# Kernel tuning notes

Hardware: AMD Instinct MI355X
Metric: run time of the kernel (lower is better)

Reference implementation:

```python
import jax, jax.numpy as jnp
import numpy as np

N_NODES = 50000
N_EDGES = 800000
D = 64
NUM_GRAPHS = 64


def gcn_conv(x, src, dst, deg_inv_sqrt, W, b):
    # GCNConv: h = X W; out_i = sum_{j->i} norm_ij * h_j + self-loop term + b
    h = x @ W  # [N, D_out]
    norm = deg_inv_sqrt[src] * deg_inv_sqrt[dst]  # [E]
    msgs = h[src] * norm[:, None]  # [E, D_out] -- dominant gather
    out = jax.ops.segment_sum(msgs, dst, num_segments=N_NODES)
    # self-loop edge (i,i) with norm = deg_i^-1
    out = out + h * (deg_inv_sqrt ** 2)[:, None]
    return out + b


def setup_inputs() -> dict:
    key = jax.random.key(0)
    ks = jax.random.split(key, 12)
    x = jax.random.normal(ks[0], (N_NODES, D), dtype=jnp.float32)
    edge_index = jax.random.randint(ks[1], (2, N_EDGES), 0, N_NODES, dtype=jnp.int64)
    batch = jnp.sort(jax.random.randint(ks[2], (N_NODES,), 0, NUM_GRAPHS, dtype=jnp.int64))
    s = 1.0 / np.sqrt(D)
    W1 = jax.random.uniform(ks[3], (D, D), jnp.float32, -s, s)
    b1 = jnp.zeros((D,), jnp.float32)
    W2 = jax.random.uniform(ks[4], (D, D), jnp.float32, -s, s)
    b2 = jnp.zeros((D,), jnp.float32)
    W3 = jax.random.uniform(ks[5], (D, D), jnp.float32, -s, s)
    b3 = jnp.zeros((D,), jnp.float32)
    Wl = jax.random.uniform(ks[6], (D, 1), jnp.float32, -s, s)
    bl = jnp.zeros((1,), jnp.float32)
    return {"x": x, "edge_index": edge_index, "batch": batch,
            "W1": W1, "b1": b1, "W2": W2, "b2": b2, "W3": W3, "b3": b3,
            "Wl": Wl, "bl": bl}


def reference(x, edge_index, batch, W1, b1, W2, b2, W3, b3, Wl, bl):
    src, dst = edge_index[0], edge_index[1]
    # symmetric GCN normalization with self-loops: deg_i = in_degree_i + 1
    deg = jax.ops.segment_sum(jnp.ones((N_EDGES,), x.dtype), dst, num_segments=N_NODES) + 1.0
    deg_inv_sqrt = deg ** -0.5
    h = jax.nn.relu(gcn_conv(x, src, dst, deg_inv_sqrt, W1, b1))
    h = jax.nn.relu(gcn_conv(h, src, dst, deg_inv_sqrt, W2, b2))
    h = jax.nn.relu(gcn_conv(h, src, dst, deg_inv_sqrt, W3, b3))
    # global mean pool over graphs
    sums = jax.ops.segment_sum(h, batch, num_segments=NUM_GRAPHS)  # [G, D]
    counts = jax.ops.segment_sum(jnp.ones((N_NODES,), h.dtype), batch, num_segments=NUM_GRAPHS)
    pooled = sums / jnp.clip(counts, 1.0)[:, None]
    return pooled @ Wl + bl  # [G, 1]
```

## Files before the change

kernel.cpp:

```cpp
#include <hip/hip_runtime.h>

#define N_NODES 50000
#define N_EDGES 800000
#define DIM 64
#define NUM_GRAPHS 64
#define NPART 8
#define PART_NODES 6250

typedef unsigned short u16;
typedef unsigned int u32;

__device__ __forceinline__ u16 bf16_rne(float f) {
  u32 u = __float_as_uint(f);
  u32 r = (u + 0x7fffu + ((u >> 16) & 1u)) >> 16;
  return (u16)r;
}

__global__ void init_kernel(int* __restrict__ cnt, float* __restrict__ partial,
                            const float* __restrict__ x, u16* __restrict__ xh) {
  int i = blockIdx.x * blockDim.x + threadIdx.x;
  if (i < N_NODES) cnt[i] = 0;
  if (i < NUM_GRAPHS) partial[i] = 0.f;
  int stride = gridDim.x * blockDim.x;
  for (int k = i; k < N_NODES * DIM / 4; k += stride) {
    float4 v = reinterpret_cast<const float4*>(x)[k];
    ushort4 o;
    o.x = bf16_rne(v.x); o.y = bf16_rne(v.y);
    o.z = bf16_rne(v.z); o.w = bf16_rne(v.w);
    reinterpret_cast<ushort4*>(xh)[k] = o;
  }
}

__global__ void pack_count_kernel(const int* __restrict__ src, const int* __restrict__ dst,
                                  u32* __restrict__ epk, int* __restrict__ cnt, int E) {
  int stride = gridDim.x * blockDim.x;
  for (int e = blockIdx.x * blockDim.x + threadIdx.x; e < E; e += stride) {
    int d = dst[e];
    int s = src[e];
    epk[e] = ((u32)s << 16) | (u32)d;
    atomicAdd(&cnt[d], 1);
  }
}

__global__ void scanA_kernel(const int* __restrict__ cnt, int* __restrict__ rowptr,
                             int* __restrict__ bsum, float* __restrict__ dis, int N) {
  __shared__ int wsum[16];
  int i = blockIdx.x * 1024 + threadIdx.x;
  int lane = threadIdx.x & 63, wid = threadIdx.x >> 6;
  int v = (i < N) ? cnt[i] : 0;
  if (i < N) dis[i] = rsqrtf((float)(v + 1));
  int sv = v;
  #pragma unroll
  for (int off = 1; off < 64; off <<= 1) {
    int t = __shfl_up(sv, off, 64);
    if (lane >= off) sv += t;
  }
  if (lane == 63) wsum[wid] = sv;
  __syncthreads();
  if (wid == 0) {
    int wv = (lane < 16) ? wsum[lane] : 0;
    #pragma unroll
    for (int off = 1; off < 16; off <<= 1) {
      int t = __shfl_up(wv, off, 64);
      if (lane >= off) wv += t;
    }
    if (lane < 16) wsum[lane] = wv;
  }
  __syncthreads();
  if (i < N) rowptr[i] = (wid ? wsum[wid - 1] : 0) + (sv - v);
  if (threadIdx.x == 1023) bsum[blockIdx.x] = wsum[15];
}

__global__ void scanC_kernel(int* __restrict__ rowptr, const int* __restrict__ bsum,
                             int* __restrict__ cursor, int nb, int N) {
  __shared__ int s_off;
  __shared__ int s_total;
  int b = blockIdx.x;
  if (threadIdx.x < 64) {
    int t = threadIdx.x;
    int v = (t < nb) ? bsum[t] : 0;
    #pragma unroll
    for (int off = 1; off < 64; off <<= 1) {
      int u = __shfl_up(v, off, 64);
      if (t >= off) v += u;
    }
    if (t == (b == 0 ? 0 : b - 1)) s_off = (b == 0) ? 0 : v;
    if (t == nb - 1) s_total = v;
  }
  __syncthreads();
  int i = b * 1024 + threadIdx.x;
  if (i < N) {
    int r = rowptr[i] + s_off;
    rowptr[i] = r;
    cursor[i] = r;
  }
  if (b == 0 && threadIdx.x == 0) rowptr[N] = s_total;
}

__global__ void fill_kernel(const u32* __restrict__ epk,
                            int* __restrict__ cursor, int* __restrict__ esrc, int E) {
  int p = blockIdx.x & 7;
  int lo = p * PART_NODES, hi = lo + PART_NODES;
  int stride = (gridDim.x >> 3) * blockDim.x;
  for (int e = (blockIdx.x >> 3) * blockDim.x + threadIdx.x; e < E; e += stride) {
    u32 rec = epk[e];
    int d = (int)(rec & 0xffffu);
    if (d >= lo && d < hi) {
      int pos = atomicAdd(&cursor[d], 1);
      esrc[pos] = (int)(rec >> 16);
    }
  }
}

#define UNPACK_FMA(q, d)                                              \
  a0 = fmaf(__uint_as_float((q).x << 16), (d), a0);                   \
  a1 = fmaf(__uint_as_float((q).x & 0xffff0000u), (d), a1);           \
  a2 = fmaf(__uint_as_float((q).y << 16), (d), a2);                   \
  a3 = fmaf(__uint_as_float((q).y & 0xffff0000u), (d), a3);           \
  a4 = fmaf(__uint_as_float((q).z << 16), (d), a4);                   \
  a5 = fmaf(__uint_as_float((q).z & 0xffff0000u), (d), a5);           \
  a6 = fmaf(__uint_as_float((q).w << 16), (d), a6);                   \
  a7 = fmaf(__uint_as_float((q).w & 0xffff0000u), (d), a7);

__global__ __launch_bounds__(256) void aggregate_kernel(const u16* __restrict__ Fh,
    const int* __restrict__ rowptr, const int* __restrict__ esrc,
    const float* __restrict__ dis, float* __restrict__ A, int N) {
  int node = blockIdx.x * 4 + (threadIdx.x >> 6);
  if (node >= N) return;
  int lane = threadIdx.x & 63;
  int qc = lane & 7;
  int qe = lane >> 3;
  const uint4* __restrict__ F8 = reinterpret_cast<const uint4*>(Fh);
  int beg = rowptr[node], end = rowptr[node + 1];
  float a0 = 0.f, a1 = 0.f, a2 = 0.f, a3 = 0.f;
  float a4 = 0.f, a5 = 0.f, a6 = 0.f, a7 = 0.f;
  int j = beg;
  for (; j + 16 <= end; j += 16) {
    int s0 = esrc[j + qe];
    int s1 = esrc[j + 8 + qe];
    float d0 = dis[s0], d1 = dis[s1];
    uint4 q0 = F8[(size_t)s0 * 8 + qc];
    uint4 q1 = F8[(size_t)s1 * 8 + qc];
    UNPACK_FMA(q0, d0)
    UNPACK_FMA(q1, d1)
  }
  if (j + 8 <= end) {
    int s0 = esrc[j + qe];
    float d0 = dis[s0];
    uint4 q0 = F8[(size_t)s0 * 8 + qc];
    UNPACK_FMA(q0, d0)
    j += 8;
  }
  if (j + qe < end) {
    int s0 = esrc[j + qe];
    float d0 = dis[s0];
    uint4 q0 = F8[(size_t)s0 * 8 + qc];
    UNPACK_FMA(q0, d0)
  }
  #pragma unroll
  for (int m = 8; m < 64; m <<= 1) {
    a0 += __shfl_xor(a0, m, 64); a1 += __shfl_xor(a1, m, 64);
    a2 += __shfl_xor(a2, m, 64); a3 += __shfl_xor(a3, m, 64);
    a4 += __shfl_xor(a4, m, 64); a5 += __shfl_xor(a5, m, 64);
    a6 += __shfl_xor(a6, m, 64); a7 += __shfl_xor(a7, m, 64);
  }
  if (qe == 0) {
    float dn = dis[node];
    uint4 qs = F8[(size_t)node * 8 + qc];
    float s0 = __uint_as_float(qs.x << 16), s1 = __uint_as_float(qs.x & 0xffff0000u);
    float s2 = __uint_as_float(qs.y << 16), s3 = __uint_as_float(qs.y & 0xffff0000u);
    float s4 = __uint_as_float(qs.z << 16), s5 = __uint_as_float(qs.z & 0xffff0000u);
    float s6 = __uint_as_float(qs.w << 16), s7 = __uint_as_float(qs.w & 0xffff0000u);
    float4 o0, o1;
    o0.x = (a0 + s0 * dn) * dn; o0.y = (a1 + s1 * dn) * dn;
    o0.z = (a2 + s2 * dn) * dn; o0.w = (a3 + s3 * dn) * dn;
    o1.x = (a4 + s4 * dn) * dn; o1.y = (a5 + s5 * dn) * dn;
    o1.z = (a6 + s6 * dn) * dn; o1.w = (a7 + s7 * dn) * dn;
    float4* A4 = reinterpret_cast<float4*>(A + (size_t)node * DIM + qc * 8);
    A4[0] = o0;
    A4[1] = o1;
  }
}

__global__ __launch_bounds__(256) void gemm_bias_relu(const float* __restrict__ X,
    const float* __restrict__ W, const float* __restrict__ b,
    u16* __restrict__ Fh, int N) {
  __shared__ float4 Xs[64][16];
  int col = threadIdx.x & 63, wid = threadIdx.x >> 6;
  float wreg[DIM];
  #pragma unroll
  for (int k = 0; k < DIM; ++k) wreg[k] = W[k * DIM + col];
  float bias = b[col];
  int row0 = blockIdx.x * 64;
  for (int i = threadIdx.x; i < 64 * 16; i += 256) {
    int r = i >> 4, c = i & 15;
    int gr = row0 + r;
    Xs[r][c] = (gr < N) ? reinterpret_cast<const float4*>(X)[(size_t)gr * 16 + c]
                        : make_float4(0.f, 0.f, 0.f, 0.f);
  }
  __syncthreads();
  for (int rr = 0; rr < 16; ++rr) {
    int lr = wid * 16 + rr;
    int row = row0 + lr;
    if (row >= N) break;
    float a0 = 0.f, a1 = 0.f, a2 = 0.f, a3 = 0.f;
    #pragma unroll
    for (int kk = 0; kk < 16; ++kk) {
      float4 xv = Xs[lr][kk];
      a0 = fmaf(xv.x, wreg[4 * kk + 0], a0);
      a1 = fmaf(xv.y, wreg[4 * kk + 1], a1);
      a2 = fmaf(xv.z, wreg[4 * kk + 2], a2);
      a3 = fmaf(xv.w, wreg[4 * kk + 3], a3);
    }
    float v = fmaxf(a0 + a1 + a2 + a3 + bias, 0.f);
    Fh[(size_t)row * DIM + col] = bf16_rne(v);
  }
}

__global__ __launch_bounds__(256) void gemm_dot_kernel(const float* __restrict__ X,
    const float* __restrict__ W, const float* __restrict__ b, const float* __restrict__ Wl,
    const int* __restrict__ batch, float* __restrict__ partial, int N) {
  __shared__ float4 Xs[64][16];
  __shared__ float yv[64];
  __shared__ float gpart[NUM_GRAPHS];
  int col = threadIdx.x & 63, wid = threadIdx.x >> 6;
  float wreg[DIM];
  #pragma unroll
  for (int k = 0; k < DIM; ++k) wreg[k] = W[k * DIM + col];
  float bias = b[col];
  float wl = Wl[col];
  int row0 = blockIdx.x * 64;
  if (threadIdx.x < 64) { yv[threadIdx.x] = 0.f; gpart[threadIdx.x] = 0.f; }
  for (int i = threadIdx.x; i < 64 * 16; i += 256) {
    int r = i >> 4, c = i & 15;
    int gr = row0 + r;
    Xs[r][c] = (gr < N) ? reinterpret_cast<const float4*>(X)[(size_t)gr * 16 + c]
                        : make_float4(0.f, 0.f, 0.f, 0.f);
  }
  __syncthreads();
  for (int rr = 0; rr < 16; ++rr) {
    int lr = wid * 16 + rr;
    int row = row0 + lr;
    if (row >= N) break;
    float a0 = 0.f, a1 = 0.f, a2 = 0.f, a3 = 0.f;
    #pragma unroll
    for (int kk = 0; kk < 16; ++kk) {
      float4 xv = Xs[lr][kk];
      a0 = fmaf(xv.x, wreg[4 * kk + 0], a0);
      a1 = fmaf(xv.y, wreg[4 * kk + 1], a1);
      a2 = fmaf(xv.z, wreg[4 * kk + 2], a2);
      a3 = fmaf(xv.w, wreg[4 * kk + 3], a3);
    }
    float v = fmaxf(a0 + a1 + a2 + a3 + bias, 0.f);
    float y = v * wl;
    #pragma unroll
    for (int off = 32; off > 0; off >>= 1) y += __shfl_down(y, off, 64);
    if (col == 0) yv[lr] = y;
  }
  __syncthreads();
  if (threadIdx.x < 64) {
    int row = row0 + threadIdx.x;
    if (row < N) atomicAdd(&gpart[batch[row]], yv[threadIdx.x]);
  }
  __syncthreads();
  if (threadIdx.x < NUM_GRAPHS) {
    int glo = batch[row0];
    int ghi = batch[min(row0 + 63, N - 1)];
    int g = threadIdx.x;
    if (g >= glo && g <= ghi) atomicAdd(&partial[g], gpart[g]);
  }
}

__global__ void pool_final_kernel(const float* __restrict__ partial, const int* __restrict__ batch,
                                  const float* __restrict__ bl, float* __restrict__ out, int N) {
  int g = threadIdx.x;
  int lo = 0, hi = N;
  while (lo < hi) { int m = (lo + hi) >> 1; if (batch[m] < g) lo = m + 1; else hi = m; }
  int start = lo;
  hi = N;
  while (lo < hi) { int m = (lo + hi) >> 1; if (batch[m] < g + 1) lo = m + 1; else hi = m; }
  float c = fmaxf((float)(lo - start), 1.f);
  out[g] = partial[g] / c + bl[0];
}

extern "C" void kernel_launch(void* const* d_in, const int* in_sizes, int n_in,
                              void* d_out, int out_size, void* d_ws, size_t ws_size,
                              hipStream_t stream) {
  const float* x     = (const float*)d_in[0];
  const int*   ei    = (const int*)d_in[1];
  const int*   batch = (const int*)d_in[2];
  const float* W1 = (const float*)d_in[3];
  const float* b1 = (const float*)d_in[4];
  const float* W2 = (const float*)d_in[5];
  const float* b2 = (const float*)d_in[6];
  const float* W3 = (const float*)d_in[7];
  const float* b3 = (const float*)d_in[8];
  const float* Wl = (const float*)d_in[9];
  const float* bl = (const float*)d_in[10];
  float* out = (float*)d_out;

  const int* srcp = ei;
  const int* dstp = ei + N_EDGES;

  char* ws = (char*)d_ws;
  size_t off = 0;
  auto alloc = [&](size_t bytes) { void* p = ws + off; off += (bytes + 255) & ~(size_t)255; return p; };
  int*   cnt     = (int*)  alloc((size_t)N_NODES * 4);
  float* dis     = (float*)alloc((size_t)N_NODES * 4);
  int*   rowptr  = (int*)  alloc((size_t)(N_NODES + 1) * 4);
  int*   bsum    = (int*)  alloc(64 * 4);
  float* partial = (float*)alloc(NUM_GRAPHS * 4);
  u32*   epk     = (u32*)  alloc((size_t)N_EDGES * 4);
  int*   esrc    = (int*)  alloc((size_t)N_EDGES * 4);
  u16*   xh      = (u16*)  alloc((size_t)N_NODES * DIM * 2);
  u16*   fh      = (u16*)  alloc((size_t)N_NODES * DIM * 2);
  float* A       = (float*)alloc((size_t)N_NODES * DIM * 4);

  const int NB = (N_NODES + 1023) / 1024;

  init_kernel<<<(N_NODES + 255) / 256, 256, 0, stream>>>(cnt, partial, x, xh);
  pack_count_kernel<<<1024, 256, 0, stream>>>(srcp, dstp, epk, cnt, N_EDGES);
  scanA_kernel<<<NB, 1024, 0, stream>>>(cnt, rowptr, bsum, dis, N_NODES);
  scanC_kernel<<<NB, 1024, 0, stream>>>(rowptr, bsum, cnt, NB, N_NODES);
  fill_kernel<<<1024, 256, 0, stream>>>(epk, cnt, esrc, N_EDGES);

  const int GB = (N_NODES + 63) / 64;
  const int AB = (N_NODES + 3) / 4;
  aggregate_kernel<<<AB, 256, 0, stream>>>(xh, rowptr, esrc, dis, A, N_NODES);
  gemm_bias_relu<<<GB, 256, 0, stream>>>(A, W1, b1, fh, N_NODES);
  aggregate_kernel<<<AB, 256, 0, stream>>>(fh, rowptr, esrc, dis, A, N_NODES);
  gemm_bias_relu<<<GB, 256, 0, stream>>>(A, W2, b2, xh, N_NODES);
  aggregate_kernel<<<AB, 256, 0, stream>>>(xh, rowptr, esrc, dis, A, N_NODES);
  gemm_dot_kernel<<<GB, 256, 0, stream>>>(A, W3, b3, Wl, batch, partial, N_NODES);
  pool_final_kernel<<<1, 64, 0, stream>>>(partial, batch, bl, out, N_NODES);
}
```

Before: 224.9 us.

## Partition aggregation by feature chunk with chunk-major output layout

The aggregate kernel now assigns each block to one of 8 feature chunks (16 bytes of bf16 each), with 16 lanes per node striding over edges, instead of one wavefront covering all 64 features of a node. Consecutive blocks take different chunks, so each chunk's slice of the feature table is gathered by its own set of blocks, which is meant to improve cache locality for the random gathers. The output is written in a chunk-major layout and the GEMM loaders read it back with adjusted indexing. The cost is that edge indices and degree values are reloaded once per chunk (8x more index traffic), reductions are shorter, and the GEMM loads from A become strided.

Result: slower. 403.1 us (+79.3%).

```diff
diff --git a/kernel.cpp b/kernel.cpp
--- a/kernel.cpp
+++ b/kernel.cpp
@@ -124,49 +124,33 @@
 
 __global__ __launch_bounds__(256) void aggregate_kernel(const u16* __restrict__ Fh,
     const int* __restrict__ rowptr, const int* __restrict__ esrc,
-    const float* __restrict__ dis, float* __restrict__ A, int N) {
-  int node = blockIdx.x * 4 + (threadIdx.x >> 6);
+    const float* __restrict__ dis, float* __restrict__ A_cm, int N) {
+  int p = blockIdx.x & 7;
+  int wid = threadIdx.x >> 6;
+  int sub = (threadIdx.x >> 4) & 3;
+  int slot = threadIdx.x & 15;
+  int node = (blockIdx.x >> 3) * 16 + wid * 4 + sub;
   if (node >= N) return;
-  int lane = threadIdx.x & 63;
-  int qc = lane & 7;
-  int qe = lane >> 3;
   const uint4* __restrict__ F8 = reinterpret_cast<const uint4*>(Fh);
   int beg = rowptr[node], end = rowptr[node + 1];
   float a0 = 0.f, a1 = 0.f, a2 = 0.f, a3 = 0.f;
   float a4 = 0.f, a5 = 0.f, a6 = 0.f, a7 = 0.f;
-  int j = beg;
-  for (; j + 16 <= end; j += 16) {
-    int s0 = esrc[j + qe];
-    int s1 = esrc[j + 8 + qe];
-    float d0 = dis[s0], d1 = dis[s1];
-    uint4 q0 = F8[(size_t)s0 * 8 + qc];
-    uint4 q1 = F8[(size_t)s1 * 8 + qc];
-    UNPACK_FMA(q0, d0)
-    UNPACK_FMA(q1, d1)
-  }
-  if (j + 8 <= end) {
-    int s0 = esrc[j + qe];
-    float d0 = dis[s0];
-    uint4 q0 = F8[(size_t)s0 * 8 + qc];
-    UNPACK_FMA(q0, d0)
-    j += 8;
-  }
-  if (j + qe < end) {
-    int s0 = esrc[j + qe];
-    float d0 = dis[s0];
-    uint4 q0 = F8[(size_t)s0 * 8 + qc];
-    UNPACK_FMA(q0, d0)
+  for (int j = beg + slot; j < end; j += 16) {
+    int s = esrc[j];
+    float d = dis[s];
+    uint4 q = F8[(size_t)s * 8 + p];
+    UNPACK_FMA(q, d)
   }
   #pragma unroll
-  for (int m = 8; m < 64; m <<= 1) {
+  for (int m = 1; m < 16; m <<= 1) {
     a0 += __shfl_xor(a0, m, 64); a1 += __shfl_xor(a1, m, 64);
     a2 += __shfl_xor(a2, m, 64); a3 += __shfl_xor(a3, m, 64);
     a4 += __shfl_xor(a4, m, 64); a5 += __shfl_xor(a5, m, 64);
     a6 += __shfl_xor(a6, m, 64); a7 += __shfl_xor(a7, m, 64);
   }
-  if (qe == 0) {
+  if (slot == 0) {
     float dn = dis[node];
-    uint4 qs = F8[(size_t)node * 8 + qc];
+    uint4 qs = F8[(size_t)node * 8 + p];
     float s0 = __uint_as_float(qs.x << 16), s1 = __uint_as_float(qs.x & 0xffff0000u);
     float s2 = __uint_as_float(qs.y << 16), s3 = __uint_as_float(qs.y & 0xffff0000u);
     float s4 = __uint_as_float(qs.z << 16), s5 = __uint_as_float(qs.z & 0xffff0000u);
@@ -176,9 +160,9 @@
     o0.z = (a2 + s2 * dn) * dn; o0.w = (a3 + s3 * dn) * dn;
     o1.x = (a4 + s4 * dn) * dn; o1.y = (a5 + s5 * dn) * dn;
     o1.z = (a6 + s6 * dn) * dn; o1.w = (a7 + s7 * dn) * dn;
-    float4* A4 = reinterpret_cast<float4*>(A + (size_t)node * DIM + qc * 8);
-    A4[0] = o0;
-    A4[1] = o1;
+    float4* outp = reinterpret_cast<float4*>(A_cm + ((size_t)p * N + node) * 8);
+    outp[0] = o0;
+    outp[1] = o1;
   }
 }
 
@@ -192,10 +176,11 @@
   for (int k = 0; k < DIM; ++k) wreg[k] = W[k * DIM + col];
   float bias = b[col];
   int row0 = blockIdx.x * 64;
+  const float4* __restrict__ A4 = reinterpret_cast<const float4*>(X);
   for (int i = threadIdx.x; i < 64 * 16; i += 256) {
     int r = i >> 4, c = i & 15;
     int gr = row0 + r;
-    Xs[r][c] = (gr < N) ? reinterpret_cast<const float4*>(X)[(size_t)gr * 16 + c]
+    Xs[r][c] = (gr < N) ? A4[((size_t)(c >> 1) * N + gr) * 2 + (c & 1)]
                         : make_float4(0.f, 0.f, 0.f, 0.f);
   }
   __syncthreads();
@@ -230,11 +215,12 @@
   float bias = b[col];
   float wl = Wl[col];
   int row0 = blockIdx.x * 64;
+  const float4* __restrict__ A4 = reinterpret_cast<const float4*>(X);
   if (threadIdx.x < 64) { yv[threadIdx.x] = 0.f; gpart[threadIdx.x] = 0.f; }
   for (int i = threadIdx.x; i < 64 * 16; i += 256) {
     int r = i >> 4, c = i & 15;
     int gr = row0 + r;
-    Xs[r][c] = (gr < N) ? reinterpret_cast<const float4*>(X)[(size_t)gr * 16 + c]
+    Xs[r][c] = (gr < N) ? A4[((size_t)(c >> 1) * N + gr) * 2 + (c & 1)]
                         : make_float4(0.f, 0.f, 0.f, 0.f);
   }
   __syncthreads();
@@ -314,7 +300,7 @@
   int*   esrc    = (int*)  alloc((size_t)N_EDGES * 4);
   u16*   xh      = (u16*)  alloc((size_t)N_NODES * DIM * 2);
   u16*   fh      = (u16*)  alloc((size_t)N_NODES * DIM * 2);
-  float* A       = (float*)alloc((size_t)N_NODES * DIM * 4);
+  float* A_cm    = (float*)alloc((size_t)NPART * N_NODES * 8 * 4);
 
   const int NB = (N_NODES + 1023) / 1024;
 
@@ -325,12 +311,12 @@
   fill_kernel<<<1024, 256, 0, stream>>>(epk, cnt, esrc, N_EDGES);
 
   const int GB = (N_NODES + 63) / 64;
-  const int AB = (N_NODES + 3) / 4;
-  aggregate_kernel<<<AB, 256, 0, stream>>>(xh, rowptr, esrc, dis, A, N_NODES);
-  gemm_bias_relu<<<GB, 256, 0, stream>>>(A, W1, b1, fh, N_NODES);
-  aggregate_kernel<<<AB, 256, 0, stream>>>(fh, rowptr, esrc, dis, A, N_NODES);
-  gemm_bias_relu<<<GB, 256, 0, stream>>>(A, W2, b2, xh, N_NODES);
-  aggregate_kernel<<<AB, 256, 0, stream>>>(xh, rowptr, esrc, dis, A, N_NODES);
-  gemm_dot_kernel<<<GB, 256, 0, stream>>>(A, W3, b3, Wl, batch, partial, N_NODES);
+  const int AB = ((N_NODES + 15) / 16) * 8;
+  aggregate_kernel<<<AB, 256, 0, stream>>>(xh, rowptr, esrc, dis, A_cm, N_NODES);
+  gemm_bias_relu<<<GB, 256, 0, stream>>>(A_cm, W1, b1, fh, N_NODES);
+  aggregate_kernel<<<AB, 256, 0, stream>>>(fh, rowptr, esrc, dis, A_cm, N_NODES);
+  gemm_bias_relu<<<GB, 256, 0, stream>>>(A_cm, W2, b2, xh, N_NODES);
+  aggregate_kernel<<<AB, 256, 0, stream>>>(xh, rowptr, esrc, dis, A_cm, N_NODES);
+  gemm_dot_kernel<<<GB, 256, 0, stream>>>(A_cm, W3, b3, Wl, batch, partial, N_NODES);
   pool_final_kernel<<<1, 64, 0, stream>>>(partial, batch, bl, out, N_NODES);
 }
```
